# Performance work log

Measured on AMD Instinct MI355X. Metric: run time of the kernel, lower is better.

The kernel has to match this reference:

```python
import jax, jax.numpy as jnp
import numpy as np
import math

B, S, D = 4, 1024, 1024
M = 32768
H = 8
HD = D // H  # 128


def setup_inputs() -> dict:
    key = jax.random.key(0)
    ks = jax.random.split(key, 7)
    return {
        "queries": jax.random.normal(ks[0], (B, S, D), dtype=jnp.float32),
        "memory_keys": jax.random.normal(ks[1], (M, D), dtype=jnp.float32),
        "memory_values": jax.random.normal(ks[2], (M, D), dtype=jnp.float32),
        "in_proj_weight": jax.random.normal(ks[3], (3 * D, D), dtype=jnp.float32) * 0.02,
        "in_proj_bias": jax.random.normal(ks[4], (3 * D,), dtype=jnp.float32) * 0.02,
        "out_proj_weight": jax.random.normal(ks[5], (D, D), dtype=jnp.float32) * 0.02,
        "out_proj_bias": jax.random.normal(ks[6], (D,), dtype=jnp.float32) * 0.02,
        "k": 16,
    }


def reference(queries, memory_keys, memory_values, in_proj_weight, in_proj_bias,
              out_proj_weight, out_proj_bias, k):
    b, s, d = queries.shape
    # similarity matmul against memory bank: [B,S,M]
    sims = jnp.einsum('bsd,md->bsm', queries, memory_keys)
    _, top_idx = jax.lax.top_k(sims, k)  # [B,S,k]
    # gather retrieved keys/values: [B,S,k,D]
    rk = memory_keys[top_idx]
    rv = memory_values[top_idx]
    # MultiheadAttention(embed_dim=D, num_heads=H) with 1 query, k kv per token
    Wq, Wk, Wv = jnp.split(in_proj_weight, 3, axis=0)
    bq, bk, bv = jnp.split(in_proj_bias, 3, axis=0)
    q = (queries @ Wq.T + bq).reshape(b, s, H, HD)
    kk = (rk @ Wk.T + bk).reshape(b, s, k, H, HD)
    vv = (rv @ Wv.T + bv).reshape(b, s, k, H, HD)
    scale = jnp.float32(1.0 / math.sqrt(HD))
    scores = jnp.einsum('bshd,bskhd->bshk', q, kk) * scale  # [B,S,H,k]
    attn = jax.nn.softmax(scores, axis=-1)
    out = jnp.einsum('bshk,bskhd->bshd', attn, vv).reshape(b, s, d)
    out = out @ out_proj_weight.T + out_proj_bias
    return out
```

## Files before the change

kernel.cpp:

```cpp
#include <hip/hip_runtime.h>
#include <hip/hip_bf16.h>

#define NROWS 4096
#define DDIM  1024
#define MKEYS 32768
#define HDIM  128
#define KSEL  16
#define NCAND 20
#define BTOP  6

#define SBM 128
#define SBN 128
#define SNKB (MKEYS / SBN)
#define CANDS_PER_ROW (SNKB * BTOP)
#define CANDS_ALLOC   2048
#define NSTEPS 16

typedef short bf16x8 __attribute__((ext_vector_type(8)));
typedef float f32x4  __attribute__((ext_vector_type(4)));

__device__ __forceinline__ float bf2f(unsigned short u) {
    union { unsigned int i; float f; } x; x.i = ((unsigned int)u) << 16; return x.f;
}
__device__ __forceinline__ unsigned short f2bf(float f) {
    union { float f; unsigned int u; } v; v.f = f;
    unsigned int r = (v.u + 0x7fffu + ((v.u >> 16) & 1u)) >> 16;
    return (unsigned short)r;
}
__device__ __forceinline__ void gload16(const void* g, const void* l) {
    __builtin_amdgcn_global_load_lds((const __attribute__((address_space(1))) unsigned int*)g,
                                     (__attribute__((address_space(3))) unsigned int*)l, 16, 0, 0);
}
template <int N>
__device__ __forceinline__ void insN(float v, int id, float* lv, int* li) {
    if (v > lv[N - 1]) {
#pragma unroll
        for (int i = 0; i < N; ++i) {
            const bool gt = v > lv[i];
            const float tv = gt ? lv[i] : v;
            const int   ti = gt ? li[i] : id;
            if (gt) { lv[i] = v; li[i] = id; }
            v = tv; id = ti;
        }
    }
}
__device__ __forceinline__ void split2(float x0, float x1, unsigned int& hp, unsigned int& lp) {
    union { float f; unsigned int u; } u0, u1;
    u0.f = x0; u1.f = x1;
    hp = (u0.u >> 16) | (u1.u & 0xffff0000u);
    const float r0 = x0 - bf2f((unsigned short)(u0.u >> 16));
    const float r1 = x1 - bf2f((unsigned short)(u1.u >> 16));
    lp = (unsigned int)f2bf(r0) | ((unsigned int)f2bf(r1) << 16);
}

__global__ __launch_bounds__(256)
void conv_bf16_kernel(const float* __restrict__ x, unsigned short* __restrict__ hi, const int n4)
{
    int i = blockIdx.x * 256 + threadIdx.x;
    const int stride = gridDim.x * 256;
    for (; i < n4; i += stride) {
        const float4 f = ((const float4*)x)[i];
        ushort4 h;
        h.x = f2bf(f.x); h.y = f2bf(f.y); h.z = f2bf(f.z); h.w = f2bf(f.w);
        ((ushort4*)hi)[i] = h;
    }
}

__global__ __launch_bounds__(256)
void split_bf16_kernel(const float* __restrict__ x, unsigned short* __restrict__ hi,
                       unsigned short* __restrict__ lo, const int n4)
{
    int i = blockIdx.x * 256 + threadIdx.x;
    const int stride = gridDim.x * 256;
    for (; i < n4; i += stride) {
        const float4 f = ((const float4*)x)[i];
        ushort4 h, l;
        h.x = f2bf(f.x); l.x = f2bf(f.x - bf2f(h.x));
        h.y = f2bf(f.y); l.y = f2bf(f.y - bf2f(h.y));
        h.z = f2bf(f.z); l.z = f2bf(f.z - bf2f(h.z));
        h.w = f2bf(f.w); l.w = f2bf(f.w - bf2f(h.w));
        ((ushort4*)hi)[i] = h;
        ((ushort4*)lo)[i] = l;
    }
}

__global__ __launch_bounds__(256)
void wk_transpose_kernel(const float* __restrict__ ipw, unsigned short* __restrict__ wkT)
{
    const int tt   = blockIdx.x * 256 + threadIdx.x;
    const int base = tt << 3;
    const int h    = base >> 17;
    const int rem  = base & 131071;
    const int j    = rem >> 7;
    const int c0   = rem & 127;
    const float* src = ipw + ((size_t)(1024 + h * 128 + c0)) * 1024 + j;
    ushort4 o0, o1;
    o0.x = f2bf(src[0]);        o0.y = f2bf(src[1024]);
    o0.z = f2bf(src[2 * 1024]); o0.w = f2bf(src[3 * 1024]);
    o1.x = f2bf(src[4 * 1024]); o1.y = f2bf(src[5 * 1024]);
    o1.z = f2bf(src[6 * 1024]); o1.w = f2bf(src[7 * 1024]);
    *(ushort4*)(wkT + base)     = o0;
    *(ushort4*)(wkT + base + 4) = o1;
}

__global__ __launch_bounds__(256)
void sims_mfma_kernel(const unsigned short* __restrict__ Qhi, const unsigned short* __restrict__ Khi,
                      float* __restrict__ cand_val, int* __restrict__ cand_idx)
{
    __shared__ char smem[32768];
    const int tid  = threadIdx.x;
    const int lane = tid & 63;
    const int w    = tid >> 6;
    const int wr   = w >> 1, wc = w & 1;
    const int row0 = blockIdx.x * SBM;
    const int key0 = blockIdx.y * SBN;

    const f32x4 zero = {0.f, 0.f, 0.f, 0.f};
    f32x4 acc[4][4];
#pragma unroll
    for (int mi = 0; mi < 4; ++mi)
#pragma unroll
        for (int ni = 0; ni < 4; ++ni) acc[mi][ni] = zero;

    const int srow = lane >> 3;
    const int scol = (((lane & 7) ^ srow) << 4);

#pragma unroll 1
    for (int step = 0; step < NSTEPS; ++step) {
        const int kbyte = step << 7;
        __syncthreads();
#pragma unroll
        for (int i = 0; i < 8; ++i) {
            const int chunk = w + (i << 2);
            const char* src;
            if (chunk < 16) {
                const int r = (chunk << 3) + srow;
                src = (const char*)Qhi + (((size_t)(row0 + r)) << 11) + kbyte + scol;
            } else {
                const int r = ((chunk - 16) << 3) + srow;
                src = (const char*)Khi + (((size_t)(key0 + r)) << 11) + kbyte + scol;
            }
            gload16(src, smem + (chunk << 10));
        }
        __syncthreads();
#pragma unroll
        for (int kk = 0; kk < 2; ++kk) {
            const int cb = (kk << 6) + ((lane >> 4) << 4);
            bf16x8 af[4], bf[4];
#pragma unroll
            for (int mi = 0; mi < 4; ++mi) {
                const int r = wr * 64 + mi * 16 + (lane & 15);
                af[mi] = *(const bf16x8*)(smem + r * 128 + (cb ^ ((r & 7) << 4)));
            }
#pragma unroll
            for (int ni = 0; ni < 4; ++ni) {
                const int r = wc * 64 + ni * 16 + (lane & 15);
                bf[ni] = *(const bf16x8*)(smem + 16384 + r * 128 + (cb ^ ((r & 7) << 4)));
            }
#pragma unroll
            for (int mi = 0; mi < 4; ++mi)
#pragma unroll
                for (int ni = 0; ni < 4; ++ni)
                    acc[mi][ni] = __builtin_amdgcn_mfma_f32_16x16x32_bf16(af[mi], bf[ni], acc[mi][ni], 0, 0, 0);
        }
    }

    float lv[BTOP]; int li[BTOP];
#pragma unroll
    for (int i = 0; i < BTOP; ++i) { lv[i] = -3.4e38f; li[i] = 0; }
    float* C_lds = (float*)smem;
    const int rowt = tid & 127;
    const int half = tid >> 7;

#pragma unroll
    for (int q = 0; q < 4; ++q) {
        __syncthreads();
        if (wc == (q >> 1)) {
#pragma unroll
            for (int mi = 0; mi < 4; ++mi)
#pragma unroll
                for (int nn = 0; nn < 2; ++nn) {
                    const int ni = ((q & 1) << 1) + nn;
                    const int r  = wr * 64 + mi * 16 + ((lane >> 4) << 2);
                    const int c  = (nn << 4) + (lane & 15);
                    const f32x4 v = acc[mi][ni];
#pragma unroll
                    for (int j = 0; j < 4; ++j) C_lds[(r + j) * 33 + c] = v[j];
                }
        }
        __syncthreads();
        const int gbase = key0 + (q << 5) + (half << 4);
#pragma unroll
        for (int cc = 0; cc < 16; ++cc)
            insN<BTOP>(C_lds[rowt * 33 + (half << 4) + cc], gbase + cc, lv, li);
    }
    __syncthreads();
    float* mv = (float*)smem;
    int*   mx = (int*)(smem + 128 * 9 * 4);
    if (half == 1) {
#pragma unroll
        for (int i = 0; i < BTOP; ++i) { mv[rowt * 9 + i] = lv[i]; mx[rowt * 9 + i] = li[i]; }
    }
    __syncthreads();
    if (half == 0) {
#pragma unroll
        for (int i = 0; i < BTOP; ++i)
            insN<BTOP>(mv[rowt * 9 + i], mx[rowt * 9 + i], lv, li);
        const size_t o = (((size_t)(row0 + rowt)) * SNKB + blockIdx.y) * BTOP;
#pragma unroll
        for (int i = 0; i < BTOP; ++i) { cand_val[o + i] = lv[i]; cand_idx[o + i] = li[i]; }
    }
}

__global__ __launch_bounds__(256)
void topk_merge_kernel(const float* __restrict__ cand_val, const int* __restrict__ cand_idx,
                       int* __restrict__ cand32)
{
    const int row  = blockIdx.x * 4 + (threadIdx.x >> 6);
    const int lane = threadIdx.x & 63;
    const size_t base = (size_t)row * CANDS_PER_ROW;
    float lv[NCAND]; int li[NCAND];
#pragma unroll
    for (int i = 0; i < NCAND; ++i) { lv[i] = -3.4e38f; li[i] = 0x7fffffff; }
#pragma unroll 1
    for (int m = 0; m < CANDS_PER_ROW / 64; ++m) {
        const int p = lane + (m << 6);
        insN<NCAND>(cand_val[base + p], cand_idx[base + p], lv, li);
    }
    int out = 0;
#pragma unroll 1
    for (int it = 0; it < NCAND; ++it) {
        float rv = lv[0]; int ridx = li[0];
#pragma unroll
        for (int off = 1; off < 64; off <<= 1) {
            const float ov = __shfl_xor(rv, off);
            const int   oi = __shfl_xor(ridx, off);
            if (ov > rv || (ov == rv && oi < ridx)) { rv = ov; ridx = oi; }
        }
        if (lane == it) out = ridx;
        if (li[0] == ridx) {
#pragma unroll
            for (int i = 0; i < NCAND - 1; ++i) { lv[i] = lv[i + 1]; li[i] = li[i + 1]; }
            lv[NCAND - 1] = -3.4e38f; li[NCAND - 1] = 0x7fffffff;
        }
    }
    if (lane < NCAND) cand32[(size_t)row * NCAND + lane] = out;
}

__global__ __launch_bounds__(256)
void rescore_kernel(const float* __restrict__ Q, const float* __restrict__ K,
                    const int* __restrict__ cand32, int* __restrict__ topk)
{
    const int row  = blockIdx.x;
    const int wv   = threadIdx.x >> 6;
    const int lane = threadIdx.x & 63;
    __shared__ float sv[NCAND];
    __shared__ int   si[NCAND];
    if (threadIdx.x < NCAND) si[threadIdx.x] = cand32[(size_t)row * NCAND + threadIdx.x];
    float4 qv[4];
#pragma unroll
    for (int u = 0; u < 4; ++u)
        qv[u] = ((const float4*)(Q + (size_t)row * DDIM))[(u << 6) + lane];
    __syncthreads();
#pragma unroll 1
    for (int c = 0; c < NCAND / 4; ++c) {
        const int slot = wv * (NCAND / 4) + c;
        const float* kr = K + (size_t)si[slot] * DDIM;
        float s = 0.f;
#pragma unroll
        for (int u = 0; u < 4; ++u) {
            const float4 kv = ((const float4*)kr)[(u << 6) + lane];
            s += kv.x * qv[u].x + kv.y * qv[u].y + kv.z * qv[u].z + kv.w * qv[u].w;
        }
#pragma unroll
        for (int off = 32; off >= 1; off >>= 1) s += __shfl_xor(s, off);
        if (lane == 0) sv[slot] = s;
    }
    __syncthreads();
    if (wv == 0) {
        float v = (lane < NCAND) ? sv[lane] : -3.4e38f;
        int  id = (lane < NCAND) ? si[lane] : 0x7fffffff;
        int out = 0;
#pragma unroll 1
        for (int it = 0; it < KSEL; ++it) {
            float rv = v; int ridx = id;
#pragma unroll
            for (int off = 1; off < 64; off <<= 1) {
                const float ov = __shfl_xor(rv, off);
                const int   oi = __shfl_xor(ridx, off);
                if (ov > rv || (ov == rv && oi < ridx)) { rv = ov; ridx = oi; }
            }
            if (lane == it) out = ridx;
            if (id == ridx) v = -3.4e38f;
        }
        if (lane < KSEL) topk[(size_t)row * KSEL + lane] = out;
    }
}

template <int LO>
__global__ __launch_bounds__(256)
void proj_split_kernel(const float* __restrict__ X, const unsigned short* __restrict__ Whi,
                       const unsigned short* __restrict__ Wlo, const float* __restrict__ bias,
                       void* __restrict__ outp, const int store_bf16)
{
    constexpr int WOFF = LO ? 32768 : 16384;
    __shared__ char smem[LO ? 65536 : 32768];
    const int tid  = threadIdx.x;
    const int lane = tid & 63;
    const int w    = tid >> 6;
    const int wr   = w >> 1, wc = w & 1;
    const int row0 = blockIdx.x * 128;
    const int col0 = blockIdx.y * 128;

    const f32x4 zero = {0.f, 0.f, 0.f, 0.f};
    f32x4 acc[4][4];
#pragma unroll
    for (int mi = 0; mi < 4; ++mi)
#pragma unroll
        for (int ni = 0; ni < 4; ++ni) acc[mi][ni] = zero;

    const int srow = lane >> 3;
    const int scol = (((lane & 7) ^ srow) << 4);
    const int xr = tid >> 1, xh = tid & 1;

    for (int step = 0; step < 16; ++step) {
        const int kbyte = step << 7;
        const int k0    = step << 6;
        __syncthreads();
#pragma unroll
        for (int i = 0; i < (LO ? 8 : 4); ++i) {
            const int chunk = w + (i << 2);
            const int plane = chunk >> 4;
            const int r     = ((chunk & 15) << 3) + srow;
            const unsigned short* Wb = plane ? Wlo : Whi;
            const char* src = (const char*)Wb + (((size_t)(col0 + r)) << 11) + kbyte + scol;
            gload16(src, smem + WOFF + (chunk << 10));
        }
        {
            const float* Xp = X + (size_t)(row0 + xr) * DDIM + k0 + xh * 32;
            float4 xa[8];
#pragma unroll
            for (int i = 0; i < 8; ++i) xa[i] = ((const float4*)Xp)[i];
            const int xbase = xr * 128;
#pragma unroll
            for (int s4 = 0; s4 < 4; ++s4) {
                const float4 a = xa[2 * s4], b = xa[2 * s4 + 1];
                uint4 hw, lw;
                if (LO) {
                    split2(a.x, a.y, hw.x, lw.x);
                    split2(a.z, a.w, hw.y, lw.y);
                    split2(b.x, b.y, hw.z, lw.z);
                    split2(b.z, b.w, hw.w, lw.w);
                } else {
                    hw.x = (unsigned int)f2bf(a.x) | ((unsigned int)f2bf(a.y) << 16);
                    hw.y = (unsigned int)f2bf(a.z) | ((unsigned int)f2bf(a.w) << 16);
                    hw.z = (unsigned int)f2bf(b.x) | ((unsigned int)f2bf(b.y) << 16);
                    hw.w = (unsigned int)f2bf(b.z) | ((unsigned int)f2bf(b.w) << 16);
                }
                const int off = xbase + ((((xh << 2) + s4) ^ (xr & 7)) << 4);
                *(uint4*)(smem + off) = hw;
                if (LO) *(uint4*)(smem + 16384 + off) = lw;
            }
        }
        asm volatile("s_waitcnt vmcnt(0)" ::: "memory");
        __syncthreads();
#pragma unroll
        for (int kk = 0; kk < 2; ++kk) {
            const int cb = (kk << 6) + ((lane >> 4) << 4);
            bf16x8 ah[4], bh[4];
#pragma unroll
            for (int mi = 0; mi < 4; ++mi) {
                const int r = wr * 64 + mi * 16 + (lane & 15);
                ah[mi] = *(const bf16x8*)(smem + r * 128 + (cb ^ ((r & 7) << 4)));
            }
#pragma unroll
            for (int ni = 0; ni < 4; ++ni) {
                const int r = wc * 64 + ni * 16 + (lane & 15);
                bh[ni] = *(const bf16x8*)(smem + WOFF + r * 128 + (cb ^ ((r & 7) << 4)));
            }
#pragma unroll
            for (int mi = 0; mi < 4; ++mi)
#pragma unroll
                for (int ni = 0; ni < 4; ++ni)
                    acc[mi][ni] = __builtin_amdgcn_mfma_f32_16x16x32_bf16(ah[mi], bh[ni], acc[mi][ni], 0, 0, 0);
            if (LO) {
                bf16x8 al[4];
#pragma unroll
                for (int mi = 0; mi < 4; ++mi) {
                    const int r = wr * 64 + mi * 16 + (lane & 15);
                    al[mi] = *(const bf16x8*)(smem + 16384 + r * 128 + (cb ^ ((r & 7) << 4)));
                }
#pragma unroll
                for (int mi = 0; mi < 4; ++mi)
#pragma unroll
                    for (int ni = 0; ni < 4; ++ni)
                        acc[mi][ni] = __builtin_amdgcn_mfma_f32_16x16x32_bf16(al[mi], bh[ni], acc[mi][ni], 0, 0, 0);
                bf16x8 bl[4];
#pragma unroll
                for (int ni = 0; ni < 4; ++ni) {
                    const int r = wc * 64 + ni * 16 + (lane & 15);
                    bl[ni] = *(const bf16x8*)(smem + WOFF + 16384 + r * 128 + (cb ^ ((r & 7) << 4)));
                }
#pragma unroll
                for (int mi = 0; mi < 4; ++mi)
#pragma unroll
                    for (int ni = 0; ni < 4; ++ni)
                        acc[mi][ni] = __builtin_amdgcn_mfma_f32_16x16x32_bf16(ah[mi], bl[ni], acc[mi][ni], 0, 0, 0);
            }
        }
    }

#pragma unroll
    for (int ni = 0; ni < 4; ++ni) {
        const int col = col0 + wc * 64 + ni * 16 + (lane & 15);
        const float bz = bias[col];
#pragma unroll
        for (int mi = 0; mi < 4; ++mi) {
            const int rbase = row0 + wr * 64 + mi * 16 + ((lane >> 4) << 2);
            const f32x4 v = acc[mi][ni];
#pragma unroll
            for (int j = 0; j < 4; ++j) {
                const float val = v[j] + bz;
                if (store_bf16)
                    ((unsigned short*)outp)[(size_t)(rbase + j) * DDIM + col] = f2bf(val);
                else
                    ((float*)outp)[(size_t)(rbase + j) * DDIM + col] = val;
            }
        }
    }
}

__global__ __launch_bounds__(256)
void ugemm_kernel(const unsigned short* __restrict__ Qpb, const unsigned short* __restrict__ wkT,
                  unsigned short* __restrict__ u)
{
    __shared__ char smem[32768];
    const int tid  = threadIdx.x;
    const int lane = tid & 63;
    const int w    = tid >> 6;
    const int wr   = w >> 1, wc = w & 1;
    const int row0 = blockIdx.x * 128;
    const int j0   = blockIdx.y * 128;
    const int h    = blockIdx.z;

    const f32x4 zero = {0.f, 0.f, 0.f, 0.f};
    f32x4 acc[4][4];
#pragma unroll
    for (int mi = 0; mi < 4; ++mi)
#pragma unroll
        for (int ni = 0; ni < 4; ++ni) acc[mi][ni] = zero;

    const int srow = lane >> 3;
    const int scol = (((lane & 7) ^ srow) << 4);

#pragma unroll 1
    for (int step = 0; step < 2; ++step) {
        const int kbyte = step << 7;
        __syncthreads();
#pragma unroll
        for (int i = 0; i < 8; ++i) {
            const int chunk = w + (i << 2);
            const char* src;
            if (chunk < 16) {
                const int r = (chunk << 3) + srow;
                src = (const char*)Qpb + (((size_t)(row0 + r)) << 11) + h * 256 + kbyte + scol;
            } else {
                const int r = ((chunk - 16) << 3) + srow;
                src = (const char*)wkT + ((size_t)h << 18) + (((size_t)(j0 + r)) << 8) + kbyte + scol;
            }
            gload16(src, smem + (chunk << 10));
        }
        __syncthreads();
#pragma unroll
        for (int kk = 0; kk < 2; ++kk) {
            const int cb = (kk << 6) + ((lane >> 4) << 4);
            bf16x8 af[4], bf[4];
#pragma unroll
            for (int mi = 0; mi < 4; ++mi) {
                const int r = wr * 64 + mi * 16 + (lane & 15);
                af[mi] = *(const bf16x8*)(smem + r * 128 + (cb ^ ((r & 7) << 4)));
            }
#pragma unroll
            for (int ni = 0; ni < 4; ++ni) {
                const int r = wc * 64 + ni * 16 + (lane & 15);
                bf[ni] = *(const bf16x8*)(smem + 16384 + r * 128 + (cb ^ ((r & 7) << 4)));
            }
#pragma unroll
            for (int mi = 0; mi < 4; ++mi)
#pragma unroll
                for (int ni = 0; ni < 4; ++ni)
                    acc[mi][ni] = __builtin_amdgcn_mfma_f32_16x16x32_bf16(af[mi], bf[ni], acc[mi][ni], 0, 0, 0);
        }
    }

#pragma unroll
    for (int ni = 0; ni < 4; ++ni) {
        const int col = j0 + wc * 64 + ni * 16 + (lane & 15);
#pragma unroll
        for (int mi = 0; mi < 4; ++mi) {
            const int rbase = row0 + wr * 64 + mi * 16 + ((lane >> 4) << 2);
            const f32x4 v = acc[mi][ni];
#pragma unroll
            for (int j = 0; j < 4; ++j)
                u[(size_t)(rbase + j) * 8192 + h * 1024 + col] = f2bf(v[j]);
        }
    }
}

__global__ __launch_bounds__(256)
void attn2_kernel(const unsigned short* __restrict__ Khi, const unsigned short* __restrict__ Vhi,
                  unsigned short* __restrict__ uz, const int* __restrict__ topk)
{
    __shared__ char smem[33344];
    int*   idx_s = (int*)(smem + 32768);
    float* sc_s  = (float*)(smem + 32832);
    const int t   = blockIdx.x;
    const int tid = threadIdx.x;
    if (tid < KSEL) idx_s[tid] = topk[(size_t)t * KSEL + tid];
    __syncthreads();
#pragma unroll
    for (int i = 0; i < 8; ++i) {
        const int s   = tid + (i << 8);
        const int row = s >> 7, col = s & 127;
        const size_t kb = ((size_t)idx_s[row]) << 11;
        gload16((const char*)Khi + kb + ((col ^ (row & 7)) << 4), smem + (s << 4));
    }
    __syncthreads();
    {
        const int p = tid >> 1, sub = tid & 1;
        const int h = p >> 4, k = p & 15;
        const unsigned short* urow = uz + (size_t)t * 8192 + h * 1024 + sub * 512;
        float s = 0.f;
#pragma unroll 8
        for (int j = 0; j < 64; ++j) {
            const uint4 uw = *(const uint4*)(urow + (j << 3));
            const uint4 kw = *(const uint4*)(smem + (k << 11) + ((((sub << 6) + j) ^ (k & 7)) << 4));
            s += bf2f((unsigned short)(uw.x & 0xffffu)) * bf2f((unsigned short)(kw.x & 0xffffu))
               + bf2f((unsigned short)(uw.x >> 16))     * bf2f((unsigned short)(kw.x >> 16))
               + bf2f((unsigned short)(uw.y & 0xffffu)) * bf2f((unsigned short)(kw.y & 0xffffu))
               + bf2f((unsigned short)(uw.y >> 16))     * bf2f((unsigned short)(kw.y >> 16))
               + bf2f((unsigned short)(uw.z & 0xffffu)) * bf2f((unsigned short)(kw.z & 0xffffu))
               + bf2f((unsigned short)(uw.z >> 16))     * bf2f((unsigned short)(kw.z >> 16))
               + bf2f((unsigned short)(uw.w & 0xffffu)) * bf2f((unsigned short)(kw.w & 0xffffu))
               + bf2f((unsigned short)(uw.w >> 16))     * bf2f((unsigned short)(kw.w >> 16));
        }
        s += __shfl_xor(s, 1);
        if (sub == 0) sc_s[h * 16 + k] = s;
    }
    __syncthreads();
#pragma unroll
    for (int i = 0; i < 8; ++i) {
        const int s   = tid + (i << 8);
        const int row = s >> 7, col = s & 127;
        const size_t kb = ((size_t)idx_s[row]) << 11;
        gload16((const char*)Vhi + kb + (col << 4), smem + (s << 4));
    }
    __syncthreads();
    const int h  = tid >> 5;
    const int dp = tid & 31;
    const float scale = 0.08838834764831845f;
    float mxv = -3.4e38f;
#pragma unroll
    for (int n = 0; n < KSEL; ++n) mxv = fmaxf(mxv, sc_s[h * 16 + n]);
    float wgt[KSEL]; float wsum = 0.f;
#pragma unroll
    for (int n = 0; n < KSEL; ++n) { wgt[n] = __expf((sc_s[h * 16 + n] - mxv) * scale); wsum += wgt[n]; }
    const float inv = 1.f / wsum;
#pragma unroll
    for (int n = 0; n < KSEL; ++n) wgt[n] *= inv;
#pragma unroll 1
    for (int j = 0; j < 16; ++j) {
        float z0 = 0.f, z1 = 0.f;
#pragma unroll
        for (int k = 0; k < 16; ++k) {
            const unsigned int vv = *(const unsigned int*)(smem + (k << 11) + (j << 7) + (dp << 2));
            z0 += wgt[k] * bf2f((unsigned short)(vv & 0xffffu));
            z1 += wgt[k] * bf2f((unsigned short)(vv >> 16));
        }
        *(unsigned int*)((char*)uz + (size_t)t * 16384 + (h << 11) + (j << 7) + (dp << 2)) =
            (unsigned int)f2bf(z0) | ((unsigned int)f2bf(z1) << 16);
    }
}

__global__ __launch_bounds__(256)
void zout_kernel(const unsigned short* __restrict__ z, const unsigned short* __restrict__ IPhi,
                 const float* __restrict__ ipb, float* __restrict__ attn_out)
{
    __shared__ char smem[32768];
    const int tid  = threadIdx.x;
    const int lane = tid & 63;
    const int w    = tid >> 6;
    const int wr   = w >> 1, wc = w & 1;
    const int row0 = blockIdx.x * 128;
    const int h    = blockIdx.y;

    const f32x4 zero = {0.f, 0.f, 0.f, 0.f};
    f32x4 acc[4][4];
#pragma unroll
    for (int mi = 0; mi < 4; ++mi)
#pragma unroll
        for (int ni = 0; ni < 4; ++ni) acc[mi][ni] = zero;

    const int srow = lane >> 3;
    const int scol = (((lane & 7) ^ srow) << 4);

#pragma unroll 1
    for (int step = 0; step < 16; ++step) {
        const int kbyte = step << 7;
        __syncthreads();
#pragma unroll
        for (int i = 0; i < 8; ++i) {
            const int chunk = w + (i << 2);
            const char* src;
            if (chunk < 16) {
                const int r = (chunk << 3) + srow;
                src = (const char*)z + (((size_t)(row0 + r)) << 14) + (h << 11) + kbyte + scol;
            } else {
                const int r = ((chunk - 16) << 3) + srow;
                src = (const char*)IPhi + (((size_t)(2048 + h * 128 + r)) << 11) + kbyte + scol;
            }
            gload16(src, smem + (chunk << 10));
        }
        __syncthreads();
#pragma unroll
        for (int kk = 0; kk < 2; ++kk) {
            const int cb = (kk << 6) + ((lane >> 4) << 4);
            bf16x8 af[4], bf[4];
#pragma unroll
            for (int mi = 0; mi < 4; ++mi) {
                const int r = wr * 64 + mi * 16 + (lane & 15);
                af[mi] = *(const bf16x8*)(smem + r * 128 + (cb ^ ((r & 7) << 4)));
            }
#pragma unroll
            for (int ni = 0; ni < 4; ++ni) {
                const int r = wc * 64 + ni * 16 + (lane & 15);
                bf[ni] = *(const bf16x8*)(smem + 16384 + r * 128 + (cb ^ ((r & 7) << 4)));
            }
#pragma unroll
            for (int mi = 0; mi < 4; ++mi)
#pragma unroll
                for (int ni = 0; ni < 4; ++ni)
                    acc[mi][ni] = __builtin_amdgcn_mfma_f32_16x16x32_bf16(af[mi], bf[ni], acc[mi][ni], 0, 0, 0);
        }
    }

#pragma unroll
    for (int ni = 0; ni < 4; ++ni) {
        const int cl = wc * 64 + ni * 16 + (lane & 15);
        const float bz = ipb[2048 + h * 128 + cl];
#pragma unroll
        for (int mi = 0; mi < 4; ++mi) {
            const int rbase = row0 + wr * 64 + mi * 16 + ((lane >> 4) << 2);
            const f32x4 v = acc[mi][ni];
#pragma unroll
            for (int j = 0; j < 4; ++j)
                attn_out[(size_t)(rbase + j) * 1024 + h * 128 + cl] = v[j] + bz;
        }
    }
}

extern "C" void kernel_launch(void* const* d_in, const int* in_sizes, int n_in,
                              void* d_out, int out_size, void* d_ws, size_t ws_size,
                              hipStream_t stream)
{
    const float* queries = (const float*)d_in[0];
    const float* mkeys   = (const float*)d_in[1];
    const float* mvals   = (const float*)d_in[2];
    const float* ipw     = (const float*)d_in[3];
    const float* ipb     = (const float*)d_in[4];
    const float* opw     = (const float*)d_in[5];
    const float* opb     = (const float*)d_in[6];

    char* ws = (char*)d_ws;
    size_t off = 0;
    auto alloc = [&](size_t bytes) -> char* {
        char* p = ws + off;
        off += (bytes + 255) & ~(size_t)255;
        return p;
    };
    unsigned short* Khi  = (unsigned short*)alloc((size_t)MKEYS * DDIM * 2);
    unsigned short* Qhi  = (unsigned short*)alloc((size_t)NROWS * DDIM * 2);
    unsigned short* IPhi = (unsigned short*)alloc((size_t)3 * DDIM * DDIM * 2);
    unsigned short* OPhi = (unsigned short*)alloc((size_t)DDIM * DDIM * 2);
    unsigned short* OPlo = (unsigned short*)alloc((size_t)DDIM * DDIM * 2);
    unsigned short* wkT  = (unsigned short*)alloc((size_t)DDIM * DDIM * 2);
    float* cand_val = (float*)alloc((size_t)NROWS * CANDS_ALLOC * 4);
    int*   cand_idx = (int*)  alloc((size_t)NROWS * CANDS_ALLOC * 4);
    int*   cand32   = (int*)  alloc((size_t)NROWS * NCAND * 4);
    int*   topk     = (int*)  alloc((size_t)NROWS * KSEL * 4);
    unsigned short* u = (unsigned short*)alloc((size_t)NROWS * 8 * DDIM * 2);
    unsigned short* Qpb = (unsigned short*)Qhi;
    unsigned short* Vhi = (unsigned short*)cand_val;
    float* attn_out     = (float*)Khi;

    conv_bf16_kernel<<<2048, 256, 0, stream>>>(queries, Qhi, NROWS * DDIM / 4);
    conv_bf16_kernel<<<2048, 256, 0, stream>>>(mkeys, Khi, MKEYS * DDIM / 4);
    conv_bf16_kernel<<<1024, 256, 0, stream>>>(ipw, IPhi, 3 * DDIM * DDIM / 4);
    split_bf16_kernel<<<512,  256, 0, stream>>>(opw, OPhi, OPlo, DDIM * DDIM / 4);
    wk_transpose_kernel<<<512, 256, 0, stream>>>(ipw, wkT);
    sims_mfma_kernel<<<dim3(NROWS / SBM, MKEYS / SBN), 256, 0, stream>>>(Qhi, Khi, cand_val, cand_idx);
    topk_merge_kernel<<<NROWS / 4, 256, 0, stream>>>(cand_val, cand_idx, cand32);
    conv_bf16_kernel<<<2048, 256, 0, stream>>>(mvals, Vhi, MKEYS * DDIM / 4);
    rescore_kernel<<<NROWS, 256, 0, stream>>>(queries, mkeys, cand32, topk);
    proj_split_kernel<0><<<dim3(NROWS / 128, 8), 256, 0, stream>>>(queries, IPhi, IPhi, ipb, Qpb, 1);
    ugemm_kernel<<<dim3(NROWS / 128, 8, 8), 256, 0, stream>>>(Qpb, wkT, u);
    attn2_kernel<<<NROWS, 256, 0, stream>>>(Khi, Vhi, u, topk);
    zout_kernel<<<dim3(NROWS / 128, 8), 256, 0, stream>>>(u, IPhi, ipb, attn_out);
    proj_split_kernel<1><<<dim3(NROWS / 128, 8), 256, 0, stream>>>(attn_out, OPhi, OPlo, opb, d_out, 0);
}
```

Before: 845.0 us.

## Drop full V bf16 conversion, gather fp32 values directly; shrink merge lists; tile transpose

Removes the pass that converts the whole 32768x1024 fp32 value bank to bf16. The attention kernel now loads only the 16 selected fp32 value rows per token and converts them to bf16 on the fly. The per-lane candidate list in the top-k merge shrinks from 20 to 8 entries, which cuts register and insertion cost but could lose true top candidates if one lane holds more than 8 of them. The Wk transpose now goes through shared memory so its global reads are coalesced.

```diff
diff --git a/kernel.cpp b/kernel.cpp
--- a/kernel.cpp
+++ b/kernel.cpp
@@ -8,6 +8,7 @@
 #define KSEL  16
 #define NCAND 20
 #define BTOP  6
+#define LCAP  8
 
 #define SBM 128
 #define SBN 128
@@ -87,20 +88,28 @@
 __global__ __launch_bounds__(256)
 void wk_transpose_kernel(const float* __restrict__ ipw, unsigned short* __restrict__ wkT)
 {
-    const int tt   = blockIdx.x * 256 + threadIdx.x;
-    const int base = tt << 3;
-    const int h    = base >> 17;
-    const int rem  = base & 131071;
-    const int j    = rem >> 7;
-    const int c0   = rem & 127;
-    const float* src = ipw + ((size_t)(1024 + h * 128 + c0)) * 1024 + j;
-    ushort4 o0, o1;
-    o0.x = f2bf(src[0]);        o0.y = f2bf(src[1024]);
-    o0.z = f2bf(src[2 * 1024]); o0.w = f2bf(src[3 * 1024]);
-    o1.x = f2bf(src[4 * 1024]); o1.y = f2bf(src[5 * 1024]);
-    o1.z = f2bf(src[6 * 1024]); o1.w = f2bf(src[7 * 1024]);
-    *(ushort4*)(wkT + base)     = o0;
-    *(ushort4*)(wkT + base + 4) = o1;
+    __shared__ unsigned short T[128 * 129];
+    const int bx  = blockIdx.x;
+    const int h   = bx >> 3, j0 = bx & 7;
+    const int tid = threadIdx.x;
+#pragma unroll 8
+    for (int i = 0; i < 64; ++i) {
+        const int idx = (i << 8) + tid;
+        const int c = idx >> 7, j = idx & 127;
+        T[c * 129 + j] = f2bf(ipw[((size_t)(1024 + h * 128 + c)) * 1024 + j0 * 128 + j]);
+    }
+    __syncthreads();
+#pragma unroll
+    for (int i = 0; i < 8; ++i) {
+        const int g  = (i << 8) + tid;
+        const int j  = g >> 4, c0 = (g & 15) << 3;
+        uint4 o;
+        o.x = (unsigned)T[(c0 + 0) * 129 + j] | ((unsigned)T[(c0 + 1) * 129 + j] << 16);
+        o.y = (unsigned)T[(c0 + 2) * 129 + j] | ((unsigned)T[(c0 + 3) * 129 + j] << 16);
+        o.z = (unsigned)T[(c0 + 4) * 129 + j] | ((unsigned)T[(c0 + 5) * 129 + j] << 16);
+        o.w = (unsigned)T[(c0 + 6) * 129 + j] | ((unsigned)T[(c0 + 7) * 129 + j] << 16);
+        *(uint4*)(wkT + ((size_t)h << 17) + ((size_t)(j0 * 128 + j) << 7) + c0) = o;
+    }
 }
 
 __global__ __launch_bounds__(256)
@@ -219,13 +228,13 @@
     const int row  = blockIdx.x * 4 + (threadIdx.x >> 6);
     const int lane = threadIdx.x & 63;
     const size_t base = (size_t)row * CANDS_PER_ROW;
-    float lv[NCAND]; int li[NCAND];
-#pragma unroll
-    for (int i = 0; i < NCAND; ++i) { lv[i] = -3.4e38f; li[i] = 0x7fffffff; }
+    float lv[LCAP]; int li[LCAP];
+#pragma unroll
+    for (int i = 0; i < LCAP; ++i) { lv[i] = -3.4e38f; li[i] = 0x7fffffff; }
 #pragma unroll 1
     for (int m = 0; m < CANDS_PER_ROW / 64; ++m) {
         const int p = lane + (m << 6);
-        insN<NCAND>(cand_val[base + p], cand_idx[base + p], lv, li);
+        insN<LCAP>(cand_val[base + p], cand_idx[base + p], lv, li);
     }
     int out = 0;
 #pragma unroll 1
@@ -240,8 +249,8 @@
         if (lane == it) out = ridx;
         if (li[0] == ridx) {
 #pragma unroll
-            for (int i = 0; i < NCAND - 1; ++i) { lv[i] = lv[i + 1]; li[i] = li[i + 1]; }
-            lv[NCAND - 1] = -3.4e38f; li[NCAND - 1] = 0x7fffffff;
+            for (int i = 0; i < LCAP - 1; ++i) { lv[i] = lv[i + 1]; li[i] = li[i + 1]; }
+            lv[LCAP - 1] = -3.4e38f; li[LCAP - 1] = 0x7fffffff;
         }
     }
     if (lane < NCAND) cand32[(size_t)row * NCAND + lane] = out;
@@ -508,7 +517,7 @@
 }
 
 __global__ __launch_bounds__(256)
-void attn2_kernel(const unsigned short* __restrict__ Khi, const unsigned short* __restrict__ Vhi,
+void attn2_kernel(const unsigned short* __restrict__ Khi, const float* __restrict__ mvals,
                   unsigned short* __restrict__ uz, const int* __restrict__ topk)
 {
     __shared__ char smem[33344];
@@ -551,9 +560,16 @@
 #pragma unroll
     for (int i = 0; i < 8; ++i) {
         const int s   = tid + (i << 8);
-        const int row = s >> 7, col = s & 127;
-        const size_t kb = ((size_t)idx_s[row]) << 11;
-        gload16((const char*)Vhi + kb + (col << 4), smem + (s << 4));
+        const int row = s >> 7, col8 = s & 127;
+        const float* vp = mvals + (((size_t)idx_s[row]) << 10) + (col8 << 3);
+        const float4 a = *(const float4*)vp;
+        const float4 b = *(const float4*)(vp + 4);
+        uint4 o;
+        o.x = (unsigned)f2bf(a.x) | ((unsigned)f2bf(a.y) << 16);
+        o.y = (unsigned)f2bf(a.z) | ((unsigned)f2bf(a.w) << 16);
+        o.z = (unsigned)f2bf(b.x) | ((unsigned)f2bf(b.y) << 16);
+        o.w = (unsigned)f2bf(b.z) | ((unsigned)f2bf(b.w) << 16);
+        *(uint4*)(smem + (s << 4)) = o;
     }
     __syncthreads();
     const int h  = tid >> 5;
@@ -690,21 +706,19 @@
     int*   topk     = (int*)  alloc((size_t)NROWS * KSEL * 4);
     unsigned short* u = (unsigned short*)alloc((size_t)NROWS * 8 * DDIM * 2);
     unsigned short* Qpb = (unsigned short*)Qhi;
-    unsigned short* Vhi = (unsigned short*)cand_val;
     float* attn_out     = (float*)Khi;
 
     conv_bf16_kernel<<<2048, 256, 0, stream>>>(queries, Qhi, NROWS * DDIM / 4);
     conv_bf16_kernel<<<2048, 256, 0, stream>>>(mkeys, Khi, MKEYS * DDIM / 4);
     conv_bf16_kernel<<<1024, 256, 0, stream>>>(ipw, IPhi, 3 * DDIM * DDIM / 4);
     split_bf16_kernel<<<512,  256, 0, stream>>>(opw, OPhi, OPlo, DDIM * DDIM / 4);
-    wk_transpose_kernel<<<512, 256, 0, stream>>>(ipw, wkT);
+    wk_transpose_kernel<<<64, 256, 0, stream>>>(ipw, wkT);
     sims_mfma_kernel<<<dim3(NROWS / SBM, MKEYS / SBN), 256, 0, stream>>>(Qhi, Khi, cand_val, cand_idx);
     topk_merge_kernel<<<NROWS / 4, 256, 0, stream>>>(cand_val, cand_idx, cand32);
-    conv_bf16_kernel<<<2048, 256, 0, stream>>>(mvals, Vhi, MKEYS * DDIM / 4);
     rescore_kernel<<<NROWS, 256, 0, stream>>>(queries, mkeys, cand32, topk);
     proj_split_kernel<0><<<dim3(NROWS / 128, 8), 256, 0, stream>>>(queries, IPhi, IPhi, ipb, Qpb, 1);
     ugemm_kernel<<<dim3(NROWS / 128, 8, 8), 256, 0, stream>>>(Qpb, wkT, u);
-    attn2_kernel<<<NROWS, 256, 0, stream>>>(Khi, Vhi, u, topk);
+    attn2_kernel<<<NROWS, 256, 0, stream>>>(Khi, mvals, u, topk);
     zout_kernel<<<dim3(NROWS / 128, 8), 256, 0, stream>>>(u, IPhi, ipb, attn_out);
     proj_split_kernel<1><<<dim3(NROWS / 128, 8), 256, 0, stream>>>(attn_out, OPhi, OPlo, opb, d_out, 0);
 }
```

New measurement: 805.8 us. 4.6% less time.
